# Optimization experiments

Measured on AMD Instinct MI355X. Metric: run time of the kernel, lower is better.

The kernel has to match this reference:

```python
import jax, jax.numpy as jnp
import numpy as np

# Spiking time schedule: B_n = (1+0.5)*X_n = 1500 per spiking layer (X_n=1000),
# chained via set_params: layer k has t_min = 1500*k, t_max = 1500*(k+1).
B_N = 1500.0


def _region_idx(H, W):
    # 0=center, 1=TL, 2=top, 3=TR, 4=right, 5=BR, 6=bottom, 7=BL, 8=left
    r = np.zeros((H, W), np.int32)
    r[0, :] = 2; r[-1, :] = 6; r[:, 0] = 8; r[:, -1] = 4
    r[0, 0] = 1; r[0, -1] = 3; r[-1, -1] = 5; r[-1, 0] = 7
    return jnp.asarray(r)


def _im2col3(x, t_min):
    # x: [B,H,W,C] -> patches [B,H,W,9*C]; 'same' pad with value t_min
    B, H, W, C = x.shape
    xp = jnp.pad(x, ((0, 0), (1, 1), (1, 1), (0, 0)), constant_values=t_min)
    cols = [xp[:, dy:dy + H, dx:dx + W, :] for dy in range(3) for dx in range(3)]
    return jnp.concatenate(cols, axis=-1)


def _spiking_conv(x, Wk, D, t_min, t_max):
    # ti = (tj - t_min) @ W + (t_max - t_min - D_region) + t_min, clamped at t_max
    p = _im2col3(x, t_min)                       # [B,H,W,9C]
    lin = jnp.einsum('bhwk,kf->bhwf', p - t_min, Wk)
    Dmap = D[_region_idx(x.shape[1], x.shape[2])]  # [H,W,F] border-aware thresholds
    return jnp.minimum(lin + (t_max - Dmap), t_max)


def _spiking_dense(x, Wk, D, t_min, t_max):
    return jnp.minimum((x - t_min) @ Wk + (t_max - D), t_max)


def _pool2(x):
    B, H, W, C = x.shape
    return x.reshape(B, H // 2, 2, W // 2, 2, C).max(axis=(2, 4))


def _forward(x, Wc1, Dc1, Wc2, Dc2, Wc3, Dc3, Wc4, Dc4, Wd1, Dd1, Wout, Dout):
    x = _spiking_conv(x, Wc1, Dc1, 0.0, 1500.0)
    x = _spiking_conv(x, Wc2, Dc2, 1500.0, 3000.0)
    x = _pool2(x)
    x = _spiking_conv(x, Wc3, Dc3, 3000.0, 4500.0)
    x = _spiking_conv(x, Wc4, Dc4, 4500.0, 6000.0)
    x = _pool2(x)
    x = x.reshape(x.shape[0], -1)                 # [B, 16*16*128]
    x = _spiking_dense(x, Wd1, Dd1, 6000.0, 7500.0)
    # output layer: alpha*(t_min - t_min_prev) + (t_min - tj)@W == D_i + (t_min - tj)@W
    return Dout + (7500.0 - x) @ Wout


def setup_inputs() -> dict:
    key = jax.random.key(0)
    ks = jax.random.split(key, 14)
    B, H, C0 = 32, 64, 1

    def w(k, fan_in, fan_out):
        return (jax.random.normal(k, (fan_in, fan_out), jnp.float32)
                / np.float32(np.sqrt(fan_in)))

    def d(k, shape):
        return jax.random.uniform(k, shape, jnp.float32) * 10.0

    return {
        'x': jax.random.uniform(ks[0], (B, H, H, C0), jnp.float32),
        'Wc1': w(ks[1], 9 * C0, 64),    'Dc1': d(ks[2], (9, 64)),
        'Wc2': w(ks[3], 9 * 64, 64),    'Dc2': d(ks[4], (9, 64)),
        'Wc3': w(ks[5], 9 * 64, 128),   'Dc3': d(ks[6], (9, 128)),
        'Wc4': w(ks[7], 9 * 128, 128),  'Dc4': d(ks[8], (9, 128)),
        'Wd1': w(ks[9], 16 * 16 * 128, 256), 'Dd1': d(ks[10], (256,)),
        'Wout': w(ks[11], 256, 10),     'Dout': d(ks[12], (10,)),
    }


def reference(x, Wc1, Dc1, Wc2, Dc2, Wc3, Dc3, Wc4, Dc4, Wd1, Dd1, Wout, Dout):
    return _forward(x, Wc1, Dc1, Wc2, Dc2, Wc3, Dc3, Wc4, Dc4, Wd1, Dd1, Wout, Dout)
```

## Files before the change

### kernel.cpp

```cpp
#include <hip/hip_runtime.h>
#include <hip/hip_bf16.h>

#define DEVINL __device__ __forceinline__

typedef __attribute__((ext_vector_type(8)))  short short8;
typedef __attribute__((ext_vector_type(4)))  float float4v;

DEVINL float bf2f(unsigned short u) { return __uint_as_float(((unsigned)u) << 16); }
DEVINL unsigned short f2bf(float f) {
  unsigned u = __float_as_uint(f);
  unsigned r = u + 0x7FFFu + ((u >> 16) & 1u);
  return (unsigned short)(r >> 16);
}
DEVINL unsigned f2bf_u(float f) { return (unsigned)f2bf(f); }

DEVINL int region_of(int h, int w, int n) {
  if (h == 0)     return (w == 0) ? 1 : ((w == n-1) ? 3 : 2);
  if (h == n-1)   return (w == 0) ? 7 : ((w == n-1) ? 5 : 6);
  return (w == 0) ? 8 : ((w == n-1) ? 4 : 0);
}

__global__ void sentinel_k(float* out, float v) {
  int t = blockIdx.x*64 + threadIdx.x;
  if (t < 320) out[t] = v;
}

__global__ void wtrans_all(const float* __restrict__ W1, const float* __restrict__ W2,
                           const float* __restrict__ W3, const float* __restrict__ W4,
                           unsigned short* __restrict__ T1, unsigned short* __restrict__ T2,
                           unsigned short* __restrict__ T3, unsigned short* __restrict__ T4)
{
  int y = blockIdx.y;
  int i = blockIdx.x*256 + threadIdx.x;
  if (y == 3) {
    if (i >= 256) return;
    int lane = i & 63, nt = i >> 6;
    int lm = lane & 15, q = lane >> 4;
    int f = nt*16 + lm;
    unsigned short v[8] = {0,0,0,0,0,0,0,0};
    if ((q & 1) == 0) {
      #pragma unroll
      for (int j = 0; j < 8; j++) v[j] = f2bf(W1[j*64 + f]);
    } else {
      v[0] = f2bf(W1[8*64 + f]);
    }
    ushort4* qq = (ushort4*)&T1[(size_t)i * 8];
    qq[0] = make_ushort4(v[0], v[1], v[2], v[3]);
    qq[1] = make_ushort4(v[4], v[5], v[6], v[7]);
    return;
  }
  const float* W = (y == 0) ? W2 : (y == 1) ? W3 : W4;
  unsigned short* T = (y == 0) ? T2 : (y == 1) ? T3 : T4;
  int Ksteps = (y == 2) ? 36 : 18;
  int NT = (y == 0) ? 4 : 8;
  int F  = (y == 0) ? 64 : 128;
  if (i >= Ksteps*NT*64) return;
  int lane = i & 63, nt = (i >> 6) % NT, kstep = i / (64*NT);
  int f = nt*16 + (lane & 15);
  int kbase = kstep*32 + (lane >> 4)*8;
  unsigned short v[8];
  #pragma unroll
  for (int j = 0; j < 8; j++) v[j] = f2bf(W[(kbase + j)*F + f]);
  ushort4* q = (ushort4*)&T[(size_t)i * 8];
  q[0] = make_ushort4(v[0], v[1], v[2], v[3]);
  q[1] = make_ushort4(v[4], v[5], v[6], v[7]);
}

__global__ __launch_bounds__(256, 4) void conv12_k(const float* __restrict__ x,
    const unsigned short* __restrict__ Wt1, const float* __restrict__ Df1,
    const unsigned short* __restrict__ Wt, const float* __restrict__ Df2,
    unsigned short* __restrict__ out)
{
  constexpr int Cpad = 72;
  __shared__ __align__(16) unsigned short u[4*66*Cpad];
  __shared__ float xs[6][66];

  int b = blockIdx.y, hp = blockIdx.x, t = threadIdx.x;
  int h0 = hp * 2;

  for (int idx = t; idx < 6*66; idx += 256) {
    int r = idx / 66, wc = idx % 66;
    int hh = h0 - 2 + r, w = wc - 1;
    float v = 0.f;
    if (hh >= 0 && hh < 64 && w >= 0 && w < 64) v = x[(b*64 + hh)*64 + w];
    xs[r][wc] = v;
  }
  {
    int r = t >> 6, c = (t >> 5) & 1, f2 = (t & 31) * 2;
    *(unsigned*)&u[(r*66 + (c ? 65 : 0))*Cpad + f2] = 0u;
  }
  __syncthreads();

  int lane = t & 63, wave = t >> 6;
  int quad = lane >> 4, lm = lane & 15;
  union ABu { float4 f4; short8 v; };
  union AW  { unsigned w32[4]; short8 v; };

  {
    short8 b1[4];
    #pragma unroll
    for (int nt = 0; nt < 4; nt++) {
      ABu tmp;
      tmp.f4 = *(const float4*)&Wt1[(size_t)((nt*64) + lane)*8];
      b1[nt] = tmp.v;
    }
    int wl = wave*16 + lm;
    bool fullq = ((quad & 1) == 0);
    bool hiq   = (quad < 2);

    for (int r = 0; r < 4; r++) {
      int hh = h0 - 1 + r;
      if (hh >= 0 && hh < 64) {
        float v[9];
        #pragma unroll
        for (int k = 0; k < 9; k++) v[k] = xs[r + k/3][wl + k%3];
        unsigned hb[9], lb[9];
        #pragma unroll
        for (int k = 0; k < 9; k++) {
          hb[k] = f2bf_u(v[k]);
          lb[k] = f2bf_u(v[k] - bf2f((unsigned short)hb[k]));
        }
        unsigned Hp[4], Lp[4];
        #pragma unroll
        for (int j = 0; j < 4; j++) {
          Hp[j] = hb[2*j] | (hb[2*j+1] << 16);
          Lp[j] = lb[2*j] | (lb[2*j+1] << 16);
        }
        AW a;
        a.w32[0] = fullq ? (hiq ? Hp[0] : Lp[0]) : (hiq ? hb[8] : lb[8]);
        a.w32[1] = fullq ? (hiq ? Hp[1] : Lp[1]) : 0u;
        a.w32[2] = fullq ? (hiq ? Hp[2] : Lp[2]) : 0u;
        a.w32[3] = fullq ? (hiq ? Hp[3] : Lp[3]) : 0u;

        float4v acc1[4];
        #pragma unroll
        for (int nt = 0; nt < 4; nt++)
          acc1[nt] = __builtin_amdgcn_mfma_f32_16x16x32_bf16(a.v, b1[nt],
                       (float4v){0.f,0.f,0.f,0.f}, 0, 0, 0);

        #pragma unroll
        for (int nt = 0; nt < 4; nt++) {
          int f = nt*16 + lm;
          #pragma unroll
          for (int reg = 0; reg < 4; reg++) {
            int w = wave*16 + quad*4 + reg;
            float val = fminf(acc1[nt][reg] - Df1[region_of(hh, w, 64)*64 + f], 0.f);
            u[(r*66 + (w+1))*Cpad + f] = f2bf(val);
          }
        }
      } else {
        #pragma unroll
        for (int nt = 0; nt < 4; nt++)
          #pragma unroll
          for (int reg = 0; reg < 4; reg++)
            u[(r*66 + (wave*16 + quad*4 + reg + 1))*Cpad + nt*16 + lm] = 0;
      }
    }
  }
  __syncthreads();

  int wm = wave >> 1, wn = wave & 1;

  float4v acc[2][2][2];
  #pragma unroll
  for (int hi = 0; hi < 2; hi++)
    #pragma unroll
    for (int m = 0; m < 2; m++)
      #pragma unroll
      for (int n = 0; n < 2; n++)
        acc[hi][m][n] = (float4v){0.f, 0.f, 0.f, 0.f};

  #pragma unroll
  for (int dy = 0; dy < 3; dy++)
  #pragma unroll
  for (int dx = 0; dx < 3; dx++)
  #pragma unroll
  for (int c0 = 0; c0 < 64; c0 += 32) {
    int kstep = (dy*3 + dx)*2 + (c0 >> 5);
    ABu bfr[2];
    #pragma unroll
    for (int n = 0; n < 2; n++)
      bfr[n].f4 = *(const float4*)&Wt[(size_t)((kstep*4 + wn*2 + n)*64 + lane)*8];
    #pragma unroll
    for (int hi = 0; hi < 2; hi++) {
      ABu afr[2];
      #pragma unroll
      for (int m = 0; m < 2; m++)
        afr[m].f4 = *(const float4*)&u[((hi+dy)*66 + ((wm*2 + m)*16 + lm + dx))*Cpad + c0 + quad*8];
      #pragma unroll
      for (int n = 0; n < 2; n++)
        #pragma unroll
        for (int m = 0; m < 2; m++)
          acc[hi][m][n] = __builtin_amdgcn_mfma_f32_16x16x32_bf16(afr[m].v, bfr[n].v, acc[hi][m][n], 0, 0, 0);
    }
  }

  #pragma unroll
  for (int m = 0; m < 2; m++)
    #pragma unroll
    for (int n = 0; n < 2; n++) {
      int mm = wm*2 + m;
      int f = (wn*2 + n)*16 + lm;
      #pragma unroll
      for (int rp = 0; rp < 2; rp++) {
        float mx = -1e30f;
        #pragma unroll
        for (int hi = 0; hi < 2; hi++)
          #pragma unroll
          for (int rr = 0; rr < 2; rr++) {
            int h = h0 + hi, w = mm*16 + quad*4 + 2*rp + rr;
            float v = fminf(acc[hi][m][n][2*rp+rr] - Df2[region_of(h, w, 64)*64 + f], 0.f);
            mx = fmaxf(mx, v);
          }
        int wp = mm*8 + quad*2 + rp;
        out[(((size_t)b*32 + hp)*32 + wp)*64 + f] = f2bf(mx);
      }
    }
}

template<int C, int F, int N, bool POOL, int FS, int MINW>
__global__ __launch_bounds__(256, MINW) void conv_mfma(
    const unsigned short* __restrict__ U, const unsigned short* __restrict__ Wt,
    const float* __restrict__ Df, unsigned short* __restrict__ out)
{
  constexpr int RC   = POOL ? 2 : 1;
  constexpr int ROWS = RC + 2;
  constexpr int Cpad = C + 8;
  constexpr int NT = F / 16;
  constexpr int MT = N / 16;
  constexpr int NTE = NT / FS;
  constexpr int MW = MT;
  constexpr int NW = NTE / 4;

  __shared__ __align__(16) unsigned short lds[ROWS*(N+2)*Cpad];

  int bx = blockIdx.x, b = blockIdx.y, t = threadIdx.x;
  int hp = bx / FS, fs = bx % FS;
  int h0 = hp * RC;

  const int stage16 = ROWS*(N+2)*(C/8);
  #pragma unroll 4
  for (int i = t; i < stage16; i += 256) {
    int c8 = i % (C/8), wc = (i/(C/8)) % (N+2), r = i/((C/8)*(N+2));
    int hh = h0 - 1 + r, w = wc - 1;
    float4 v = make_float4(0.f,0.f,0.f,0.f);
    if (hh >= 0 && hh < N && w >= 0 && w < N)
      v = *(const float4*)&U[(((size_t)b*N + hh)*N + w)*C + c8*8];
    *(float4*)&lds[(r*(N+2) + wc)*Cpad + c8*8] = v;
  }
  __syncthreads();

  int lane = t & 63, wave = t >> 6;
  int wn = wave;
  int quad = lane >> 4, lm = lane & 15;

  union ABu { float4 f4; short8 v; };

  float4v acc[RC][MW][NW];
  #pragma unroll
  for (int hi = 0; hi < RC; hi++)
    #pragma unroll
    for (int m = 0; m < MW; m++)
      #pragma unroll
      for (int n = 0; n < NW; n++)
        acc[hi][m][n] = (float4v){0.f, 0.f, 0.f, 0.f};

  #pragma unroll
  for (int dy = 0; dy < 3; dy++)
  #pragma unroll
  for (int dx = 0; dx < 3; dx++)
  #pragma unroll
  for (int c0 = 0; c0 < C; c0 += 32) {
    int kstep = (dy*3 + dx)*(C/32) + (c0 >> 5);
    ABu bfr[NW];
    #pragma unroll
    for (int n = 0; n < NW; n++)
      bfr[n].f4 = *(const float4*)&Wt[(size_t)((kstep*NT + fs*NTE + wn*NW + n)*64 + lane)*8];
    #pragma unroll
    for (int hi = 0; hi < RC; hi++) {
      ABu afr[MW];
      #pragma unroll
      for (int m = 0; m < MW; m++)
        afr[m].f4 = *(const float4*)&lds[((hi+dy)*(N+2) + (m*16 + lm + dx))*Cpad + c0 + quad*8];
      #pragma unroll
      for (int n = 0; n < NW; n++)
        #pragma unroll
        for (int m = 0; m < MW; m++)
          acc[hi][m][n] = __builtin_amdgcn_mfma_f32_16x16x32_bf16(afr[m].v, bfr[n].v, acc[hi][m][n], 0, 0, 0);
    }
  }

  if constexpr (POOL) {
    constexpr int M2 = N/2;
    #pragma unroll
    for (int m = 0; m < MW; m++)
      #pragma unroll
      for (int n = 0; n < NW; n++) {
        int f = (fs*NTE + wn*NW + n)*16 + lm;
        #pragma unroll
        for (int rp = 0; rp < 2; rp++) {
          float mx = -1e30f;
          #pragma unroll
          for (int hi = 0; hi < 2; hi++)
            #pragma unroll
            for (int rr = 0; rr < 2; rr++) {
              int h = h0 + hi, w = m*16 + quad*4 + 2*rp + rr;
              float v = fminf(acc[hi][m][n][2*rp+rr] - Df[region_of(h, w, N)*F + f], 0.f);
              mx = fmaxf(mx, v);
            }
          int wp = m*8 + quad*2 + rp;
          out[(((size_t)b*M2 + hp)*M2 + wp)*F + f] = f2bf(mx);
        }
      }
  } else {
    int h = h0;
    #pragma unroll
    for (int m = 0; m < MW; m++)
      #pragma unroll
      for (int n = 0; n < NW; n++) {
        int f = (fs*NTE + wn*NW + n)*16 + lm;
        #pragma unroll
        for (int r = 0; r < 4; r++) {
          int w = m*16 + quad*4 + r;
          int reg = region_of(h, w, N);
          float v = fminf(acc[0][m][n][r] - Df[reg*F + f], 0.f);
          out[(((size_t)b*N + h)*N + w)*F + f] = f2bf(v);
        }
      }
  }
}

__global__ __launch_bounds__(256) void dense_k(const unsigned short* __restrict__ act,
    const float* __restrict__ W, float* __restrict__ part)
{
  int blk = blockIdx.x, t = threadIdx.x;
  int kblk = blk >> 1, fh = blk & 1;
  int k0 = kblk * 128;
  __shared__ float a[128][36];
  for (int idx = t; idx < 32*128; idx += 256) {
    int bb = idx >> 7, kc = idx & 127;
    a[kc][bb] = bf2f(act[(size_t)bb*32768 + k0 + kc]);
  }
  __syncthreads();
  int f0 = fh*128 + (t & 31)*4, b0 = (t >> 5)*4;
  float acc[4][4] = {};
  #pragma unroll 8
  for (int kc = 0; kc < 128; kc++) {
    float4 wv = *(const float4*)&W[(size_t)(k0 + kc)*256 + f0];
    float4 av = *(const float4*)&a[kc][b0];
    const float* avp = (const float*)&av;
    #pragma unroll
    for (int bb = 0; bb < 4; bb++) {
      float avx = avp[bb];
      acc[bb][0] += avx * wv.x;
      acc[bb][1] += avx * wv.y;
      acc[bb][2] += avx * wv.z;
      acc[bb][3] += avx * wv.w;
    }
  }
  #pragma unroll
  for (int bb = 0; bb < 4; bb++) {
    float4 v = make_float4(acc[bb][0], acc[bb][1], acc[bb][2], acc[bb][3]);
    *(float4*)&part[(size_t)kblk*8192 + (b0+bb)*256 + f0] = v;
  }
}

__global__ __launch_bounds__(1024) void redfin_k(const float* __restrict__ part,
    const float* __restrict__ Dd, const float* __restrict__ Wo,
    const float* __restrict__ Do, float* __restrict__ out)
{
  int b = blockIdx.x, t = threadIdx.x;
  int f = t & 255, kq = t >> 8;
  float s = 0.f;
  #pragma unroll 16
  for (int blk = kq*64; blk < kq*64 + 64; blk++)
    s += part[(size_t)blk*8192 + b*256 + f];
  __shared__ float red[4][256];
  red[kq][f] = s;
  __syncthreads();
  __shared__ float ud[256];
  if (t < 256) {
    float v = red[0][t] + red[1][t] + red[2][t] + red[3][t];
    ud[t] = fminf(v - Dd[t], 0.f);
  }
  __syncthreads();
  int lane = t & 63, wave = t >> 6;
  if (wave < 4) {
    for (int o = wave; o < 10; o += 4) {
      float acc = 0.f;
      #pragma unroll
      for (int j = 0; j < 4; j++) {
        int ff = j*64 + lane;
        acc += ud[ff] * Wo[ff*10 + o];
      }
      #pragma unroll
      for (int off = 32; off; off >>= 1) acc += __shfl_down(acc, off, 64);
      if (lane == 0) out[b*10 + o] = Do[o] - acc;
    }
  }
}

extern "C" void kernel_launch(void* const* d_in, const int* in_sizes, int n_in,
                              void* d_out, int out_size, void* d_ws, size_t ws_size,
                              hipStream_t stream)
{
  float* outp = (float*)d_out;

  if (n_in != 13) { sentinel_k<<<5, 64, 0, stream>>>(outp, 200.f); return; }
  const int exp_sz[13] = {131072, 576, 576, 36864, 576, 73728, 1152,
                          147456, 1152, 8388608, 256, 2560, 10};
  for (int i = 0; i < 13; i++)
    if (in_sizes[i] != exp_sz[i]) {
      sentinel_k<<<5, 64, 0, stream>>>(outp, 1000.f + 100.f*i); return;
    }
  if (ws_size < (37u << 20)) { sentinel_k<<<5, 64, 0, stream>>>(outp, 500.f); return; }

  char* wsb = (char*)d_ws;
  const float* x    = (const float*)d_in[0];
  const float* Wc1  = (const float*)d_in[1];
  const float* Dc1  = (const float*)d_in[2];
  const float* Wc2  = (const float*)d_in[3];
  const float* Dc2  = (const float*)d_in[4];
  const float* Wc3  = (const float*)d_in[5];
  const float* Dc3  = (const float*)d_in[6];
  const float* Wc4  = (const float*)d_in[7];
  const float* Dc4  = (const float*)d_in[8];
  const float* Wd1  = (const float*)d_in[9];
  const float* Dd1  = (const float*)d_in[10];
  const float* Wout = (const float*)d_in[11];
  const float* Dout = (const float*)d_in[12];

  unsigned short* Wt2 = (unsigned short*)(wsb + (1u << 20));
  unsigned short* Wt3 = (unsigned short*)(wsb + (1u << 20) + 262144);
  unsigned short* Wt4 = (unsigned short*)(wsb + (1u << 20) + 524288);
  unsigned short* Wt1 = (unsigned short*)(wsb + (1u << 20) + 921600);
  unsigned short* P2  = (unsigned short*)(wsb + (19u << 20));
  unsigned short* U3  = (unsigned short*)(wsb + (2u  << 20));
  unsigned short* P4  = (unsigned short*)(wsb + (25u << 20));
  float* part         = (float*)(wsb + (2u  << 20));

  wtrans_all<<<dim3(72, 4), 256, 0, stream>>>(Wc1, Wc2, Wc3, Wc4, Wt1, Wt2, Wt3, Wt4);
  conv12_k<<<dim3(32, 32), 256, 0, stream>>>(x, Wt1, Dc1, Wt2, Dc2, P2);
  conv_mfma<64, 128, 32, false, 1, 2><<<dim3(32, 32), 256, 0, stream>>>(P2, Wt3, Dc3, U3);
  conv_mfma<128, 128, 32, true, 2, 4><<<dim3(32, 32), 256, 0, stream>>>(U3, Wt4, Dc4, P4);
  dense_k<<<512, 256, 0, stream>>>(P4, Wd1, part);
  redfin_k<<<32, 1024, 0, stream>>>(part, Dd1, Wout, Dout, outp);
}
```

Baseline: 154.1 us.

## Add dedicated conv4 kernel with two-row tiles and fused 2x2 pooling

Replaces the generic templated MFMA conv for layer 4 with a specialized kernel in which each block computes two output rows and max-pools them directly. Three input rows are staged in LDS, while the second output row's shifted input row is read directly from global memory inside the MFMA loop. This aims to cut per-block overhead and LDS staging. It risks uncoalesced, bounds-checked global loads in the inner loop and half as many blocks.

```diff
diff --git a/kernel.cpp b/kernel.cpp
--- a/kernel.cpp
+++ b/kernel.cpp
@@ -328,6 +328,105 @@
         }
       }
   }
+}
+
+__global__ __launch_bounds__(256, 2) void conv4_k(
+    const unsigned short* __restrict__ U, const unsigned short* __restrict__ Wt,
+    const float* __restrict__ Df, unsigned short* __restrict__ out)
+{
+  constexpr int C = 128, Cpad = 136, N = 32;
+  __shared__ __align__(16) unsigned short lds[3*34*Cpad];
+
+  int b = blockIdx.y, hp = blockIdx.x, t = threadIdx.x;
+  int h0 = hp * 2;
+
+  const int stage16 = 3*34*(C/8);
+  #pragma unroll 4
+  for (int i = t; i < stage16; i += 256) {
+    int c8 = i % 16, wc = (i/16) % 34, r = i/(16*34);
+    int hh = h0 - 1 + r, w = wc - 1;
+    float4 v = make_float4(0.f,0.f,0.f,0.f);
+    if (hh >= 0 && hh < N && w >= 0 && w < N)
+      v = *(const float4*)&U[(((size_t)b*N + hh)*N + w)*C + c8*8];
+    *(float4*)&lds[(r*34 + wc)*Cpad + c8*8] = v;
+  }
+  __syncthreads();
+
+  int lane = t & 63, wave = t >> 6;
+  int wn = wave, quad = lane >> 4, lm = lane & 15;
+  union ABu { float4 f4; short8 v; };
+
+  float4v acc[2][2][2];
+  #pragma unroll
+  for (int hi = 0; hi < 2; hi++)
+    #pragma unroll
+    for (int m = 0; m < 2; m++)
+      #pragma unroll
+      for (int n = 0; n < 2; n++)
+        acc[hi][m][n] = (float4v){0.f, 0.f, 0.f, 0.f};
+
+  #pragma unroll
+  for (int dy = 0; dy < 3; dy++)
+  #pragma unroll
+  for (int dx = 0; dx < 3; dx++)
+  #pragma unroll
+  for (int c0 = 0; c0 < C; c0 += 32) {
+    int kstep = (dy*3 + dx)*4 + (c0 >> 5);
+    ABu bfr[2];
+    #pragma unroll
+    for (int n = 0; n < 2; n++)
+      bfr[n].f4 = *(const float4*)&Wt[(size_t)((kstep*8 + wn*2 + n)*64 + lane)*8];
+
+    ABu afr0[2];
+    #pragma unroll
+    for (int m = 0; m < 2; m++)
+      afr0[m].f4 = *(const float4*)&lds[(dy*34 + (m*16 + lm + dx))*Cpad + c0 + quad*8];
+
+    ABu afr1[2];
+    {
+      int h1 = h0 + dy;
+      #pragma unroll
+      for (int m = 0; m < 2; m++) {
+        int wo = m*16 + lm + dx - 1;
+        float4 av = make_float4(0.f,0.f,0.f,0.f);
+        if (h1 < N && wo >= 0 && wo < N)
+          av = *(const float4*)&U[(((size_t)b*N + h1)*N + wo)*C + c0 + quad*8];
+        afr1[m].f4 = av;
+      }
+    }
+
+    #pragma unroll
+    for (int n = 0; n < 2; n++)
+      #pragma unroll
+      for (int m = 0; m < 2; m++)
+        acc[0][m][n] = __builtin_amdgcn_mfma_f32_16x16x32_bf16(afr0[m].v, bfr[n].v, acc[0][m][n], 0, 0, 0);
+    #pragma unroll
+    for (int n = 0; n < 2; n++)
+      #pragma unroll
+      for (int m = 0; m < 2; m++)
+        acc[1][m][n] = __builtin_amdgcn_mfma_f32_16x16x32_bf16(afr1[m].v, bfr[n].v, acc[1][m][n], 0, 0, 0);
+  }
+
+  #pragma unroll
+  for (int m = 0; m < 2; m++)
+    #pragma unroll
+    for (int n = 0; n < 2; n++) {
+      int f = (wn*2 + n)*16 + lm;
+      #pragma unroll
+      for (int rp = 0; rp < 2; rp++) {
+        float mx = -1e30f;
+        #pragma unroll
+        for (int hi = 0; hi < 2; hi++)
+          #pragma unroll
+          for (int rr = 0; rr < 2; rr++) {
+            int h = h0 + hi, w = m*16 + quad*4 + 2*rp + rr;
+            float v = fminf(acc[hi][m][n][2*rp+rr] - Df[region_of(h, w, N)*128 + f], 0.f);
+            mx = fmaxf(mx, v);
+          }
+        int wp = m*8 + quad*2 + rp;
+        out[(((size_t)b*16 + hp)*16 + wp)*128 + f] = f2bf(mx);
+      }
+    }
 }
 
 __global__ __launch_bounds__(256) void dense_k(const unsigned short* __restrict__ act,
@@ -442,7 +541,7 @@
   wtrans_all<<<dim3(72, 4), 256, 0, stream>>>(Wc1, Wc2, Wc3, Wc4, Wt1, Wt2, Wt3, Wt4);
   conv12_k<<<dim3(32, 32), 256, 0, stream>>>(x, Wt1, Dc1, Wt2, Dc2, P2);
   conv_mfma<64, 128, 32, false, 1, 2><<<dim3(32, 32), 256, 0, stream>>>(P2, Wt3, Dc3, U3);
-  conv_mfma<128, 128, 32, true, 2, 4><<<dim3(32, 32), 256, 0, stream>>>(U3, Wt4, Dc4, P4);
+  conv4_k<<<dim3(16, 32), 256, 0, stream>>>(U3, Wt4, Dc4, P4);
   dense_k<<<512, 256, 0, stream>>>(P4, Wd1, part);
   redfin_k<<<32, 1024, 0, stream>>>(part, Dd1, Wout, Dout, outp);
 }
```

After: 162.5 us. 1.05x slower.
